# Performance work log

Measured on AMD Instinct MI355X. Metric: run time of the kernel, lower is better.

Reference implementation:

```python
import jax, jax.numpy as jnp
import numpy as np

B, T, D, H, L = 8, 64, 128, 4, 4
G = B * T            # 512 frame-graphs
NPG = 200            # nodes per graph
N = G * NPG          # 102400 nodes
E = 8 * N            # 819200 edges
FIN, HID = 2, 64
DH = D // H
NCLS = 2


def setup_inputs():
    key = jax.random.key(0)
    ks = jax.random.split(key, 16)
    w = lambda k, s: (jax.random.normal(k, s) * 0.05).astype(jnp.float32)
    x = jax.random.normal(ks[0], (N, FIN), dtype=jnp.float32)
    g = jax.random.randint(ks[1], (E,), 0, G)
    src = (g * NPG + jax.random.randint(ks[2], (E,), 0, NPG)).astype(jnp.int32)
    dst = (g * NPG + jax.random.randint(ks[3], (E,), 0, NPG)).astype(jnp.int32)
    node_graph = (jnp.arange(N) // NPG).astype(jnp.int32)
    return dict(
        x=x, edge_src=src, edge_dst=dst, node_graph=node_graph,
        gW1=w(ks[4], (FIN, HID)), gb1=jnp.zeros((HID,), jnp.float32),
        ln1g=jnp.ones((HID,), jnp.float32), ln1b=jnp.zeros((HID,), jnp.float32),
        gW2=w(ks[5], (HID, HID)), gb2=jnp.zeros((HID,), jnp.float32),
        ln2g=jnp.ones((HID,), jnp.float32), ln2b=jnp.zeros((HID,), jnp.float32),
        gW3=w(ks[6], (HID, D)), gb3=jnp.zeros((D,), jnp.float32),
        tWqkv=w(ks[7], (L, 3 * D, D)), tbqkv=jnp.zeros((L, 3 * D), jnp.float32),
        tWo=w(ks[8], (L, D, D)), tbo=jnp.zeros((L, D), jnp.float32),
        tg1=jnp.ones((L, D), jnp.float32), tb1=jnp.zeros((L, D), jnp.float32),
        tg2=jnp.ones((L, D), jnp.float32), tb2=jnp.zeros((L, D), jnp.float32),
        tWf1=w(ks[9], (L, 4 * D, D)), tbf1=jnp.zeros((L, 4 * D), jnp.float32),
        tWf2=w(ks[10], (L, D, 4 * D)), tbf2=jnp.zeros((L, D), jnp.float32),
        hW1=w(ks[11], (D // 2, D)), hb1=jnp.zeros((D // 2,), jnp.float32),
        hW2=w(ks[12], (NCLS, D // 2)), hb2=jnp.zeros((NCLS,), jnp.float32),
    )


def _ln(x, g, b, eps=1e-5):
    m = jnp.mean(x, -1, keepdims=True)
    v = jnp.var(x, -1, keepdims=True)
    return (x - m) * jax.lax.rsqrt(v + eps) * g + b


def _forward(x, edge_src, edge_dst, node_graph, gW1, gb1, ln1g, ln1b, gW2, gb2,
             ln2g, ln2b, gW3, gb3, tWqkv, tbqkv, tWo, tbo, tg1, tb1, tg2, tb2,
             tWf1, tbf1, tWf2, tbf2, hW1, hb1, hW2, hb2):
    # --- GCN encoder (PyG GCNConv: sym-normalized A with self loops) ---
    loops = jnp.arange(N, dtype=jnp.int32)
    src = jnp.concatenate([edge_src, loops])
    dst = jnp.concatenate([edge_dst, loops])
    deg = jnp.zeros((N,), x.dtype).at[dst].add(1.0)
    dinv = jax.lax.rsqrt(deg)
    norm = (dinv[src] * dinv[dst])[:, None]

    def gcn(h, W, b):
        h = h @ W  # transform first (smaller message dim when FIN < HID)
        return jax.ops.segment_sum(h[src] * norm, dst, num_segments=N) + b

    h = _ln(jax.nn.relu(gcn(x, gW1, gb1)), ln1g, ln1b)
    h = _ln(jax.nn.relu(gcn(h, gW2, gb2)), ln2g, ln2b)
    h = gcn(h, gW3, gb3)  # (N, D)

    # per-graph mean readout (replaces the python loop in the original)
    cnt = jax.ops.segment_sum(jnp.ones((N,), h.dtype), node_graph, num_segments=G)
    emb = jax.ops.segment_sum(h, node_graph, num_segments=G) / cnt[:, None]
    seq = emb.reshape(B, T, D)

    # --- sinusoidal positional encoding ---
    pos = jnp.arange(T, dtype=jnp.float32)[:, None]
    div = jnp.exp(jnp.arange(0, D, 2, dtype=jnp.float32) * (-np.log(10000.0) / D))
    pe = jnp.zeros((T, D), jnp.float32)
    pe = pe.at[:, 0::2].set(jnp.sin(pos * div)).at[:, 1::2].set(jnp.cos(pos * div))
    seq = seq + pe

    # --- TransformerEncoder (post-norm, relu FFN, batch_first) ---
    scale = 1.0 / np.sqrt(DH)
    for l in range(L):
        qkv = seq @ tWqkv[l].T + tbqkv[l]
        q, k, v = jnp.split(qkv, 3, axis=-1)
        q = q.reshape(B, T, H, DH).transpose(0, 2, 1, 3)
        k = k.reshape(B, T, H, DH).transpose(0, 2, 1, 3)
        v = v.reshape(B, T, H, DH).transpose(0, 2, 1, 3)
        att = jax.nn.softmax(jnp.einsum('bhqd,bhkd->bhqk', q, k) * scale, axis=-1)
        a = jnp.einsum('bhqk,bhkd->bhqd', att, v).transpose(0, 2, 1, 3).reshape(B, T, D)
        seq = _ln(seq + a @ tWo[l].T + tbo[l], tg1[l], tb1[l])
        f = jax.nn.relu(seq @ tWf1[l].T + tbf1[l]) @ tWf2[l].T + tbf2[l]
        seq = _ln(seq + f, tg2[l], tb2[l])

    pooled = jnp.mean(seq, axis=1)  # mask=None path -> plain temporal mean
    return jax.nn.relu(pooled @ hW1.T + hb1) @ hW2.T + hb2  # (B, NCLS)


def reference(x, edge_src, edge_dst, node_graph, gW1, gb1, ln1g, ln1b, gW2, gb2,
              ln2g, ln2b, gW3, gb3, tWqkv, tbqkv, tWo, tbo, tg1, tb1, tg2, tb2,
              tWf1, tbf1, tWf2, tbf2, hW1, hb1, hW2, hb2):
    return _forward(x, edge_src, edge_dst, node_graph, gW1, gb1, ln1g, ln1b,
                    gW2, gb2, ln2g, ln2b, gW3, gb3, tWqkv, tbqkv, tWo, tbo,
                    tg1, tb1, tg2, tb2, tWf1, tbf1, tWf2, tbf2, hW1, hb1, hW2, hb2)
```

## Files before the change

kernel.cpp:

```cpp
#include <hip/hip_runtime.h>

#define NN   102400
#define EE   819200
#define GG   512
#define NPG  200
#define DD   128
#define TT   64
#define BB   8
#define LL   4
#define ECHUNK 12800
#define SCAP 2560
#define NSLOT 16

typedef unsigned int uint;

static __device__ __forceinline__ void wave_sum64_2(float& a, float& b) {
#pragma unroll
    for (int off = 32; off > 0; off >>= 1) {
        a += __shfl_xor(a, off, 64);
        b += __shfl_xor(b, off, 64);
    }
}


__global__ __launch_bounds__(256) void k_a1(const int* __restrict__ src,
                                            int* __restrict__ hist) {
    __shared__ int h[GG];
    int tid = threadIdx.x;
    h[tid] = 0; h[tid + 256] = 0;
    __syncthreads();
    int base = blockIdx.x * ECHUNK;
#pragma unroll 2
    for (int it = 0; it < 50; ++it)
        atomicAdd(&h[src[base + it * 256 + tid] / NPG], 1);
    __syncthreads();
    hist[blockIdx.x * GG + tid] = h[tid];
    hist[blockIdx.x * GG + tid + 256] = h[tid + 256];
}

__global__ __launch_bounds__(512) void k_a2(const int* __restrict__ hist,
                                            int* __restrict__ off2,
                                            int* __restrict__ goff) {
    __shared__ int sm[GG];
    int g = threadIdx.x;
    int s = 0;
    for (int b = 0; b < 64; ++b) s += hist[b * GG + g];
    sm[g] = s;
    __syncthreads();
    for (int d = 1; d < GG; d <<= 1) {
        int v = (g >= d) ? sm[g - d] : 0;
        __syncthreads();
        sm[g] += v;
        __syncthreads();
    }
    int base = sm[g] - s;
    goff[g] = base;
    if (g == GG - 1) goff[GG] = sm[g];
    int run = base;
    for (int b = 0; b < 64; ++b) {
        off2[b * GG + g] = run;
        run += hist[b * GG + g];
    }
}

__global__ __launch_bounds__(256) void k_a3(const int* __restrict__ src,
                                            const int* __restrict__ dst,
                                            const int* __restrict__ off2,
                                            uint* __restrict__ gpack) {
    __shared__ int cur[GG];
    int tid = threadIdx.x;
    cur[tid] = off2[blockIdx.x * GG + tid];
    cur[tid + 256] = off2[blockIdx.x * GG + tid + 256];
    __syncthreads();
    int base = blockIdx.x * ECHUNK;
    for (int it = 0; it < 50; ++it) {
        int e = base + it * 256 + tid;
        int s = src[e], d = dst[e];
        int g = s / NPG;
        int pos = atomicAdd(&cur[g], 1);
        gpack[pos] = ((uint)(s - g * NPG) << 8) | (uint)(d - g * NPG);
    }
}

__global__ __launch_bounds__(256) void k_bsort(
    const float* __restrict__ x, const int* __restrict__ goff,
    const uint* __restrict__ gpack, const float* __restrict__ W1,
    const float* __restrict__ gb1, const float* __restrict__ lng,
    const float* __restrict__ lnb, uint2* __restrict__ slots,
    uint2* __restrict__ ovf, int* __restrict__ ovfcnt,
    float* __restrict__ wgtv, float* __restrict__ hout) {
    int g = ((blockIdx.x & 7) << 6) | (blockIdx.x >> 3);
    __shared__ float2 xs[NPG];
    __shared__ float2 aggl[NPG];
    __shared__ int cnt2[NPG];
    __shared__ int lnoff[NPG + 1];
    __shared__ int cur[NPG];
    __shared__ float rsq[NPG];
    __shared__ float cwl[NPG];
    __shared__ uint srec[SCAP];
    __shared__ int sm[256];
    __shared__ uint2 ovfl[128];
    __shared__ int ovfcur;
    int tid = threadIdx.x;
    int base = goff[g], E = goff[g + 1] - base;
    const float2* x2 = (const float2*)x;
    if (tid < NPG) { xs[tid] = x2[g * NPG + tid]; cnt2[tid] = 0; cwl[tid] = 0.f; }
    if (tid == 0) ovfcur = 0;
    __syncthreads();
    for (int i = tid; i < E; i += 256) atomicAdd(&cnt2[gpack[base + i] & 255u], 1);
    __syncthreads();
    int c = (tid < NPG) ? cnt2[tid] : 0;
    sm[tid] = c;
    __syncthreads();
    for (int d = 1; d < 256; d <<= 1) {
        int v = (tid >= d) ? sm[tid - d] : 0;
        __syncthreads();
        sm[tid] += v;
        __syncthreads();
    }
    if (tid < NPG) {
        lnoff[tid] = sm[tid] - c;
        cur[tid] = sm[tid] - c;
        rsq[tid] = rsqrtf((float)(c + 1));
    }
    if (tid == 0) lnoff[NPG] = E;
    __syncthreads();
    for (int i = tid; i < E; i += 256) {
        uint r = gpack[base + i];
        int pos = atomicAdd(&cur[r & 255u], 1);
        srec[pos] = r;
    }
    __syncthreads();
    for (int i = tid; i < E; i += 256) {
        uint r = srec[i];
        atomicAdd(&cwl[r >> 8], rsq[r >> 8] * rsq[r & 255u]);
    }
    __syncthreads();
    if (tid < NPG) {
        int e0 = lnoff[tid], En = lnoff[tid + 1] - e0;
        float rd = rsq[tid];
        float dv = rd * rd;
        uint2* op = &slots[(size_t)(g * NPG + tid) * NSLOT];
        op[0] = make_uint2((uint)(g * NPG + tid), __float_as_uint(dv));
        float ax = xs[tid].x * dv, ay = xs[tid].y * dv;
#pragma unroll
        for (int s = 1; s < NSLOT; ++s) {
            uint2 v;
            if (s - 1 < En) {
                uint r = srec[e0 + s - 1];
                int ls = r >> 8;
                float w = rsq[ls] * rd;
                v = make_uint2((uint)(g * NPG + ls), __float_as_uint(w));
                ax += xs[ls].x * w;
                ay += xs[ls].y * w;
            } else {
                v = make_uint2((uint)(g * NPG + tid), 0u);
            }
            op[s] = v;
        }
        for (int e = NSLOT - 1; e < En; ++e) {
            uint r = srec[e0 + e];
            int ls = r >> 8;
            float w = rsq[ls] * rd;
            ax += xs[ls].x * w;
            ay += xs[ls].y * w;
            int p = atomicAdd(&ovfcur, 1);
            if (p < 128)
                ovfl[p] = make_uint2(((uint)tid << 17) | (uint)(g * NPG + ls),
                                     __float_as_uint(w));
        }
        aggl[tid] = make_float2(ax, ay);
        wgtv[g * NPG + tid] = cwl[tid] + dv;
    }
    __syncthreads();
    int nov = ovfcur < 128 ? ovfcur : 128;
    if (tid == 0) ovfcnt[g] = nov;
    if (tid < nov) ovf[g * 128 + tid] = ovfl[tid];
    int lane = tid & 63, wid = tid >> 6;
    float w0 = W1[lane], w1 = W1[64 + lane];
    float gbj = gb1[lane], lgj = lng[lane], lbj = lnb[lane];
    for (int i = wid; i < NPG; i += 4) {
        float2 a = aggl[i];
        float u = fmaxf(a.x * w0 + a.y * w1 + gbj, 0.f);
        float s2 = u, q2 = u * u;
        wave_sum64_2(s2, q2);
        float mean = s2 * (1.f / 64.f);
        float var = q2 * (1.f / 64.f) - mean * mean;
        hout[(size_t)(g * NPG + i) * 64 + lane] = (u - mean) * rsqrtf(var + 1e-5f) * lgj + lbj;
    }
}


__global__ __launch_bounds__(256) void k_agg_lin_ln(
    const float* __restrict__ t, const float* __restrict__ W,
    const float* __restrict__ gb, const float* __restrict__ lng,
    const float* __restrict__ lnb, const uint2* __restrict__ slots,
    const uint2* __restrict__ ovf, const int* __restrict__ ovfcnt,
    float* __restrict__ hout) {
    int c = ((blockIdx.x & 7) << 8) | (blockIdx.x >> 3);
    int n0 = c * 50;
    int g = c >> 2, lbase = (c & 3) * 50;
    __shared__ float hs[50][64];
    __shared__ uint2 slt[50][NSLOT];
    int tid = threadIdx.x, lane = tid & 63, wid = tid >> 6;
    int grp = lane >> 4, fq = lane & 15;
    {
        const float4* s4 = (const float4*)&slots[(size_t)n0 * NSLOT];
        float4* d4 = (float4*)slt;
        for (int i = tid; i < 50 * NSLOT / 2; i += 256) d4[i] = s4[i];
    }
    __syncthreads();
    for (int i = wid; i < 50; i += 4) {
        float4 acc = make_float4(0.f, 0.f, 0.f, 0.f);
#pragma unroll
        for (int r = 0; r < 4; ++r) {
            uint2 s = slt[i][r * 4 + grp];
            float w = __uint_as_float(s.y);
            float4 tv = *(const float4*)&t[(size_t)s.x * 64 + fq * 4];
            acc.x += tv.x * w; acc.y += tv.y * w;
            acc.z += tv.z * w; acc.w += tv.w * w;
        }
        acc.x += __shfl_xor(acc.x, 16); acc.y += __shfl_xor(acc.y, 16);
        acc.z += __shfl_xor(acc.z, 16); acc.w += __shfl_xor(acc.w, 16);
        acc.x += __shfl_xor(acc.x, 32); acc.y += __shfl_xor(acc.y, 32);
        acc.z += __shfl_xor(acc.z, 32); acc.w += __shfl_xor(acc.w, 32);
        if (grp == 0) *(float4*)&hs[i][fq * 4] = acc;
    }
    __syncthreads();
    int nov = ovfcnt[g];
    if (nov && wid == 0) {
        for (int k = 0; k < nov; ++k) {
            uint2 r = ovf[g * 128 + k];
            int ld = r.x >> 17;
            if (ld >= lbase && ld < lbase + 50)
                hs[ld - lbase][lane] +=
                    t[(size_t)(r.x & 0x1FFFFu) * 64 + lane] * __uint_as_float(r.y);
        }
    }
    __syncthreads();
    float wreg[64];
#pragma unroll
    for (int k = 0; k < 64; ++k) wreg[k] = W[k * 64 + lane];
    float gbj = gb[lane], lgj = lng[lane], lbj = lnb[lane];
    for (int i = wid; i < 50; i += 4) {
        const float4* hrow = (const float4*)&hs[i][0];
        float a0 = 0.f, a1 = 0.f;
#pragma unroll
        for (int k4 = 0; k4 < 16; k4 += 2) {
            float4 h0 = hrow[k4], h1 = hrow[k4 + 1];
            a0 += h0.x * wreg[4 * k4] + h0.y * wreg[4 * k4 + 1] +
                  h0.z * wreg[4 * k4 + 2] + h0.w * wreg[4 * k4 + 3];
            a1 += h1.x * wreg[4 * k4 + 4] + h1.y * wreg[4 * k4 + 5] +
                  h1.z * wreg[4 * k4 + 6] + h1.w * wreg[4 * k4 + 7];
        }
        float u = fmaxf(a0 + a1 + gbj, 0.f);
        float s = u, q = u * u;
        wave_sum64_2(s, q);
        float mean = s * (1.f / 64.f);
        float var = q * (1.f / 64.f) - mean * mean;
        hout[(size_t)(n0 + i) * 64 + lane] = (u - mean) * rsqrtf(var + 1e-5f) * lgj + lbj;
    }
}

__global__ __launch_bounds__(256) void k_wpool_emb(
    const float* __restrict__ h2, const float* __restrict__ wgtv,
    const float* __restrict__ W3, const float* __restrict__ b3,
    float* __restrict__ seq) {
    int g = ((blockIdx.x & 7) << 6) | (blockIdx.x >> 3);
    int n0 = g * NPG;
    __shared__ float wgt[NPG];
    __shared__ float red[4][64];
    __shared__ float ps[64];
    int tid = threadIdx.x, lane = tid & 63, wid = tid >> 6;
    for (int i = tid; i < NPG; i += 256) wgt[i] = wgtv[n0 + i];
    __syncthreads();
    float acc = 0.f;
    for (int i = wid; i < NPG; i += 4)
        acc += h2[(size_t)(n0 + i) * 64 + lane] * wgt[i];
    red[wid][lane] = acc;
    __syncthreads();
    if (tid < 64)
        ps[tid] = (red[0][tid] + red[1][tid] + red[2][tid] + red[3][tid]) * (1.f / NPG);
    __syncthreads();
    if (tid < 128) {
        int d = tid;
        float a = b3[d];
#pragma unroll 8
        for (int k = 0; k < 64; ++k) a += ps[k] * W3[k * DD + d];
        float freq = expf((float)(d & ~1) * (-9.210340371976184f / 128.f));
        float ang = (float)(g & (TT - 1)) * freq;
        a += (d & 1) ? cosf(ang) : sinf(ang);
        seq[(size_t)g * DD + d] = a;
    }
}


__global__ __launch_bounds__(512) void k_qkv_attn(
    const float* __restrict__ seq, const float* __restrict__ Wqkv,
    const float* __restrict__ bqkv, float* __restrict__ abuf) {
    int b = blockIdx.x >> 2, h = blockIdx.x & 3;
    __shared__ float seqs[64][132];
    __shared__ float Qs[64][36], Ks[64][36], Vs[64][36];
    __shared__ float Ss[64][68];
    int tid = threadIdx.x;
    for (int i = tid; i < 64 * 32; i += 512) {
        int r = i >> 5, c = i & 31;
        float4 v = *(const float4*)&seq[(size_t)(b * 64 + r) * DD + c * 4];
        *(float4*)&seqs[r][c * 4] = v;
    }
    __syncthreads();
    {
        int r = tid & 63, jg = tid >> 6;
        float acc[12];
        int wrow[12];
#pragma unroll
        for (int i = 0; i < 12; ++i) {
            int jj = jg * 12 + i;
            int row = (jj < 32) ? (h * 32 + jj)
                    : (jj < 64) ? (128 + h * 32 + jj - 32)
                                : (256 + h * 32 + jj - 64);
            wrow[i] = row;
            acc[i] = bqkv[row];
        }
        for (int kc = 0; kc < 8; ++kc) {
            float4 s0 = *(const float4*)&seqs[r][kc * 16 + 0];
            float4 s1 = *(const float4*)&seqs[r][kc * 16 + 4];
            float4 s2 = *(const float4*)&seqs[r][kc * 16 + 8];
            float4 s3 = *(const float4*)&seqs[r][kc * 16 + 12];
#pragma unroll
            for (int i = 0; i < 12; ++i) {
                const float4* wp = (const float4*)&Wqkv[(size_t)wrow[i] * DD + kc * 16];
                float4 w0 = wp[0], w1 = wp[1], w2 = wp[2], w3 = wp[3];
                acc[i] += s0.x * w0.x + s0.y * w0.y + s0.z * w0.z + s0.w * w0.w +
                          s1.x * w1.x + s1.y * w1.y + s1.z * w1.z + s1.w * w1.w +
                          s2.x * w2.x + s2.y * w2.y + s2.z * w2.z + s2.w * w2.w +
                          s3.x * w3.x + s3.y * w3.y + s3.z * w3.z + s3.w * w3.w;
            }
        }
#pragma unroll
        for (int i = 0; i < 12; ++i) {
            int jj = jg * 12 + i;
            if (jj < 32) Qs[r][jj] = acc[i];
            else if (jj < 64) Ks[r][jj - 32] = acc[i];
            else Vs[r][jj - 64] = acc[i];
        }
    }
    __syncthreads();
    int q = tid >> 3, kg = tid & 7;
    const float scale = 0.17677669529663687f;
    float p[8];
    float mx = -1e30f;
#pragma unroll
    for (int kk = 0; kk < 8; ++kk) {
        int k = kg * 8 + kk;
        float a = 0.f;
#pragma unroll
        for (int dq = 0; dq < 8; ++dq) {
            float4 qv = *(const float4*)&Qs[q][dq * 4];
            float4 kv = *(const float4*)&Ks[k][dq * 4];
            a += qv.x * kv.x + qv.y * kv.y + qv.z * kv.z + qv.w * kv.w;
        }
        p[kk] = a * scale;
        mx = fmaxf(mx, p[kk]);
    }
    mx = fmaxf(mx, __shfl_xor(mx, 1));
    mx = fmaxf(mx, __shfl_xor(mx, 2));
    mx = fmaxf(mx, __shfl_xor(mx, 4));
    float ssum = 0.f;
#pragma unroll
    for (int kk = 0; kk < 8; ++kk) {
        p[kk] = expf(p[kk] - mx);
        ssum += p[kk];
    }
    ssum += __shfl_xor(ssum, 1);
    ssum += __shfl_xor(ssum, 2);
    ssum += __shfl_xor(ssum, 4);
    float inv = 1.f / ssum;
#pragma unroll
    for (int kk = 0; kk < 8; ++kk) Ss[q][kg * 8 + kk] = p[kk] * inv;
    __syncthreads();
    float4 o = make_float4(0.f, 0.f, 0.f, 0.f);
    for (int k = 0; k < 64; ++k) {
        float pw = Ss[q][k];
        float4 v = *(const float4*)&Vs[k][kg * 4];
        o.x += pw * v.x; o.y += pw * v.y; o.z += pw * v.z; o.w += pw * v.w;
    }
    *(float4*)&abuf[(size_t)(b * 64 + q) * DD + h * 32 + kg * 4] = o;
}

__global__ __launch_bounds__(128) void k_proj_ln(
    const float* __restrict__ abuf, const float* __restrict__ Wo,
    const float* __restrict__ bo, const float* __restrict__ g,
    const float* __restrict__ bl, float* __restrict__ seq) {
    int m = blockIdx.x, tid = threadIdx.x;
    __shared__ float arow[128];
    __shared__ float sred[2][2];
    arow[tid] = abuf[(size_t)m * DD + tid];
    __syncthreads();
    float acc = bo[tid];
    const float4* wr = (const float4*)&Wo[(size_t)tid * DD];
    const float4* ar = (const float4*)arow;
#pragma unroll
    for (int k = 0; k < 32; ++k) {
        float4 w = wr[k], a = ar[k];
        acc += a.x * w.x + a.y * w.y + a.z * w.z + a.w * w.w;
    }
    float u = seq[(size_t)m * DD + tid] + acc;
    float s = u, q2 = u * u;
    wave_sum64_2(s, q2);
    int wid = tid >> 6;
    if ((tid & 63) == 0) { sred[wid][0] = s; sred[wid][1] = q2; }
    __syncthreads();
    s = sred[0][0] + sred[1][0];
    q2 = sred[0][1] + sred[1][1];
    float mean = s * (1.f / 128.f);
    float var = q2 * (1.f / 128.f) - mean * mean;
    float rstd = rsqrtf(var + 1e-5f);
    seq[(size_t)m * DD + tid] = (u - mean) * rstd * g[tid] + bl[tid];
}

__global__ __launch_bounds__(256) void k_ffn_ln(
    const float* __restrict__ Wf1, const float* __restrict__ bf1,
    const float* __restrict__ Wf2, const float* __restrict__ bf2,
    const float* __restrict__ g, const float* __restrict__ bl,
    float* __restrict__ seq) {
    int m0 = blockIdx.x * 2, tid = threadIdx.x;
    __shared__ float srow[2][128];
    __shared__ float f1[2][512];
    __shared__ float pf[2][128];
    __shared__ float sred2[2][4];
    {
        int rr = tid >> 7, d = tid & 127;
        srow[rr][d] = seq[(size_t)(m0 + rr) * DD + d];
    }
    __syncthreads();
    const float4* s0 = (const float4*)srow[0];
    const float4* s1 = (const float4*)srow[1];
#pragma unroll
    for (int rep = 0; rep < 2; ++rep) {
        int o = tid + rep * 256;
        float bv = bf1[o];
        float a0 = bv, a1 = bv;
        const float4* wr = (const float4*)&Wf1[(size_t)o * DD];
#pragma unroll
        for (int k = 0; k < 32; ++k) {
            float4 w = wr[k];
            float4 x0 = s0[k], x1 = s1[k];
            a0 += x0.x * w.x + x0.y * w.y + x0.z * w.z + x0.w * w.w;
            a1 += x1.x * w.x + x1.y * w.y + x1.z * w.z + x1.w * w.w;
        }
        f1[0][o] = fmaxf(a0, 0.f);
        f1[1][o] = fmaxf(a1, 0.f);
    }
    __syncthreads();
    int d = tid & 127, half = tid >> 7;
    float b0 = half ? 0.f : bf2[d];
    float a0 = b0, a1 = b0;
    const float4* wr2 = (const float4*)&Wf2[(size_t)d * 512 + half * 256];
    const float4* f10 = (const float4*)&f1[0][half * 256];
    const float4* f11 = (const float4*)&f1[1][half * 256];
#pragma unroll
    for (int k = 0; k < 64; ++k) {
        float4 w = wr2[k];
        float4 x0 = f10[k], x1 = f11[k];
        a0 += x0.x * w.x + x0.y * w.y + x0.z * w.z + x0.w * w.w;
        a1 += x1.x * w.x + x1.y * w.y + x1.z * w.z + x1.w * w.w;
    }
    if (half) { pf[0][d] = a0; pf[1][d] = a1; }
    __syncthreads();
    float u0 = 0.f, u1 = 0.f;
    if (half == 0) {
        u0 = srow[0][d] + a0 + pf[0][d];
        u1 = srow[1][d] + a1 + pf[1][d];
        float s0_ = u0, q0_ = u0 * u0, s1_ = u1, q1_ = u1 * u1;
        wave_sum64_2(s0_, q0_);
        wave_sum64_2(s1_, q1_);
        int w_ = d >> 6;
        if ((d & 63) == 0) {
            sred2[w_][0] = s0_; sred2[w_][1] = q0_;
            sred2[w_][2] = s1_; sred2[w_][3] = q1_;
        }
    }
    __syncthreads();
    if (half == 0) {
        float S0 = sred2[0][0] + sred2[1][0], Q0 = sred2[0][1] + sred2[1][1];
        float S1 = sred2[0][2] + sred2[1][2], Q1 = sred2[0][3] + sred2[1][3];
        float mean0 = S0 * (1.f / 128.f);
        float var0 = Q0 * (1.f / 128.f) - mean0 * mean0;
        float rstd0 = rsqrtf(var0 + 1e-5f);
        float mean1 = S1 * (1.f / 128.f);
        float var1 = Q1 * (1.f / 128.f) - mean1 * mean1;
        float rstd1 = rsqrtf(var1 + 1e-5f);
        seq[(size_t)m0 * DD + d] = (u0 - mean0) * rstd0 * g[d] + bl[d];
        seq[(size_t)(m0 + 1) * DD + d] = (u1 - mean1) * rstd1 * g[d] + bl[d];
    }
}

__global__ __launch_bounds__(128) void k_head(
    const float* __restrict__ seq, const float* __restrict__ W1,
    const float* __restrict__ b1, const float* __restrict__ W2,
    const float* __restrict__ b2, float* __restrict__ out) {
    int b = blockIdx.x, t = threadIdx.x;
    __shared__ float pooled[DD];
    __shared__ float hid[64];
    float s = 0.f;
    for (int i = 0; i < TT; ++i) s += seq[(size_t)(b * TT + i) * DD + t];
    pooled[t] = s * (1.f / TT);
    __syncthreads();
    if (t < 64) {
        float a = b1[t];
        const float* wr = W1 + t * DD;
        for (int k = 0; k < DD; ++k) a += pooled[k] * wr[k];
        hid[t] = fmaxf(a, 0.f);
    }
    __syncthreads();
    if (t < 2) {
        float a = b2[t];
        const float* wr = W2 + t * 64;
        for (int k = 0; k < 64; ++k) a += hid[k] * wr[k];
        out[b * 2 + t] = a;
    }
}


extern "C" void kernel_launch(void* const* d_in, const int* in_sizes, int n_in,
                              void* d_out, int out_size, void* d_ws, size_t ws_size,
                              hipStream_t stream) {
    const float* x     = (const float*)d_in[0];
    const int*   esrc  = (const int*)d_in[1];
    const int*   edst  = (const int*)d_in[2];
    const float* gW1   = (const float*)d_in[4];
    const float* gb1   = (const float*)d_in[5];
    const float* ln1g  = (const float*)d_in[6];
    const float* ln1b  = (const float*)d_in[7];
    const float* gW2   = (const float*)d_in[8];
    const float* gb2   = (const float*)d_in[9];
    const float* ln2g  = (const float*)d_in[10];
    const float* ln2b  = (const float*)d_in[11];
    const float* gW3   = (const float*)d_in[12];
    const float* gb3   = (const float*)d_in[13];
    const float* tWqkv = (const float*)d_in[14];
    const float* tbqkv = (const float*)d_in[15];
    const float* tWo   = (const float*)d_in[16];
    const float* tbo   = (const float*)d_in[17];
    const float* tg1   = (const float*)d_in[18];
    const float* tb1   = (const float*)d_in[19];
    const float* tg2   = (const float*)d_in[20];
    const float* tb2   = (const float*)d_in[21];
    const float* tWf1  = (const float*)d_in[22];
    const float* tbf1  = (const float*)d_in[23];
    const float* tWf2  = (const float*)d_in[24];
    const float* tbf2  = (const float*)d_in[25];
    const float* hW1   = (const float*)d_in[26];
    const float* hb1   = (const float*)d_in[27];
    const float* hW2   = (const float*)d_in[28];
    const float* hb2   = (const float*)d_in[29];
    float* out = (float*)d_out;

    int*   hist   = (int*)d_ws;
    int*   off2   = hist + 64 * GG;
    int*   goff   = off2 + 64 * GG;
    uint*  gpack  = (uint*)(goff + 516);
    uint2* slots  = (uint2*)(gpack + EE);
    uint2* ovf    = slots + (size_t)NN * NSLOT;
    int*   ovfcnt = (int*)(ovf + GG * 128);
    float* wgtv   = (float*)(ovfcnt + GG);
    float* bufA = wgtv + NN;
    float* bufB = bufA + (size_t)NN * 64;
    float* seq  = bufB + (size_t)NN * 64;
    float* abuf = seq + GG * DD;

    k_a1<<<64, 256, 0, stream>>>(esrc, hist);
    k_a2<<<1, 512, 0, stream>>>(hist, off2, goff);
    k_a3<<<64, 256, 0, stream>>>(esrc, edst, off2, gpack);
    k_bsort<<<GG, 256, 0, stream>>>(x, goff, gpack, gW1, gb1, ln1g, ln1b,
                                    slots, ovf, ovfcnt, wgtv, bufA);

    k_agg_lin_ln<<<NN / 50, 256, 0, stream>>>(bufA, gW2, gb2, ln2g, ln2b,
                                              slots, ovf, ovfcnt, bufB);
    k_wpool_emb<<<GG, 256, 0, stream>>>(bufB, wgtv, gW3, gb3, seq);

    for (int l = 0; l < LL; l++) {
        k_qkv_attn<<<BB * 4, 512, 0, stream>>>(
            seq, tWqkv + (size_t)l * 384 * 128, tbqkv + l * 384, abuf);
        k_proj_ln<<<GG, 128, 0, stream>>>(
            abuf, tWo + (size_t)l * 128 * 128, tbo + l * 128,
            tg1 + l * 128, tb1 + l * 128, seq);
        k_ffn_ln<<<GG / 2, 256, 0, stream>>>(
            tWf1 + (size_t)l * 512 * 128, tbf1 + l * 512,
            tWf2 + (size_t)l * 128 * 512, tbf2 + l * 128,
            tg2 + l * 128, tb2 + l * 128, seq);
    }

    k_head<<<BB, DD, 0, stream>>>(seq, hW1, hb1, hW2, hb2, out);
}
```

Measured before the change: 392.8 us.

## Fuse attention output projection+LN into FFN+LN kernel per layer

Merges the per-row output-projection/residual/LayerNorm kernel into the FFN kernel, so each block of two rows computes Wo projection, LN1, FFN and LN2 without writing the intermediate seq to global memory. This removes one launch per transformer layer and a global round trip of the seq activations. It also adds a min-blocks occupancy hint to the GCN aggregation kernel. The second __syncthreads moves inside divergent if/else branches, which relies on AMD barrier semantics across branches.

```diff
diff --git a/kernel.cpp b/kernel.cpp
--- a/kernel.cpp
+++ b/kernel.cpp
@@ -191,7 +191,7 @@
 }
 
 
-__global__ __launch_bounds__(256) void k_agg_lin_ln(
+__global__ __launch_bounds__(256, 4) void k_agg_lin_ln(
     const float* __restrict__ t, const float* __restrict__ W,
     const float* __restrict__ gb, const float* __restrict__ lng,
     const float* __restrict__ lnb, const uint2* __restrict__ slots,
@@ -388,50 +388,45 @@
     *(float4*)&abuf[(size_t)(b * 64 + q) * DD + h * 32 + kg * 4] = o;
 }
 
-__global__ __launch_bounds__(128) void k_proj_ln(
+__global__ __launch_bounds__(256) void k_post(
     const float* __restrict__ abuf, const float* __restrict__ Wo,
-    const float* __restrict__ bo, const float* __restrict__ g,
-    const float* __restrict__ bl, float* __restrict__ seq) {
-    int m = blockIdx.x, tid = threadIdx.x;
-    __shared__ float arow[128];
-    __shared__ float sred[2][2];
-    arow[tid] = abuf[(size_t)m * DD + tid];
-    __syncthreads();
-    float acc = bo[tid];
-    const float4* wr = (const float4*)&Wo[(size_t)tid * DD];
-    const float4* ar = (const float4*)arow;
-#pragma unroll
-    for (int k = 0; k < 32; ++k) {
-        float4 w = wr[k], a = ar[k];
-        acc += a.x * w.x + a.y * w.y + a.z * w.z + a.w * w.w;
-    }
-    float u = seq[(size_t)m * DD + tid] + acc;
-    float s = u, q2 = u * u;
-    wave_sum64_2(s, q2);
-    int wid = tid >> 6;
-    if ((tid & 63) == 0) { sred[wid][0] = s; sred[wid][1] = q2; }
-    __syncthreads();
-    s = sred[0][0] + sred[1][0];
-    q2 = sred[0][1] + sred[1][1];
-    float mean = s * (1.f / 128.f);
-    float var = q2 * (1.f / 128.f) - mean * mean;
-    float rstd = rsqrtf(var + 1e-5f);
-    seq[(size_t)m * DD + tid] = (u - mean) * rstd * g[tid] + bl[tid];
-}
-
-__global__ __launch_bounds__(256) void k_ffn_ln(
-    const float* __restrict__ Wf1, const float* __restrict__ bf1,
-    const float* __restrict__ Wf2, const float* __restrict__ bf2,
-    const float* __restrict__ g, const float* __restrict__ bl,
-    float* __restrict__ seq) {
+    const float* __restrict__ bo, const float* __restrict__ g1,
+    const float* __restrict__ bl1, const float* __restrict__ Wf1,
+    const float* __restrict__ bf1, const float* __restrict__ Wf2,
+    const float* __restrict__ bf2, const float* __restrict__ g2,
+    const float* __restrict__ bl2, float* __restrict__ seq) {
     int m0 = blockIdx.x * 2, tid = threadIdx.x;
+    __shared__ float arow[2][128];
     __shared__ float srow[2][128];
     __shared__ float f1[2][512];
     __shared__ float pf[2][128];
+    __shared__ float sred[4][2];
     __shared__ float sred2[2][4];
+    int rr = tid >> 7, d0 = tid & 127;
+    arow[rr][d0] = abuf[(size_t)(m0 + rr) * DD + d0];
+    __syncthreads();
     {
-        int rr = tid >> 7, d = tid & 127;
-        srow[rr][d] = seq[(size_t)(m0 + rr) * DD + d];
+        float acc = bo[d0];
+        const float4* wr = (const float4*)&Wo[(size_t)d0 * DD];
+        const float4* ar = (const float4*)arow[rr];
+#pragma unroll
+        for (int k = 0; k < 32; ++k) {
+            float4 w = wr[k], a = ar[k];
+            acc += a.x * w.x + a.y * w.y + a.z * w.z + a.w * w.w;
+        }
+        float u = seq[(size_t)(m0 + rr) * DD + d0] + acc;
+        float s = u, q = u * u;
+        wave_sum64_2(s, q);
+        int wv = tid >> 6;
+        if ((tid & 63) == 0) { sred[wv][0] = s; sred[wv][1] = q; }
+        __syncthreads();
+        int wp = rr * 2;
+        s = sred[wp][0] + sred[wp + 1][0];
+        q = sred[wp][1] + sred[wp + 1][1];
+        float mean = s * (1.f / 128.f);
+        float var = q * (1.f / 128.f) - mean * mean;
+        float rstd = rsqrtf(var + 1e-5f);
+        srow[rr][d0] = (u - mean) * rstd * g1[d0] + bl1[d0];
     }
     __syncthreads();
     const float4* s0 = (const float4*)srow[0];
@@ -468,10 +463,9 @@
     }
     if (half) { pf[0][d] = a0; pf[1][d] = a1; }
     __syncthreads();
-    float u0 = 0.f, u1 = 0.f;
     if (half == 0) {
-        u0 = srow[0][d] + a0 + pf[0][d];
-        u1 = srow[1][d] + a1 + pf[1][d];
+        float u0 = srow[0][d] + a0 + pf[0][d];
+        float u1 = srow[1][d] + a1 + pf[1][d];
         float s0_ = u0, q0_ = u0 * u0, s1_ = u1, q1_ = u1 * u1;
         wave_sum64_2(s0_, q0_);
         wave_sum64_2(s1_, q1_);
@@ -480,9 +474,7 @@
             sred2[w_][0] = s0_; sred2[w_][1] = q0_;
             sred2[w_][2] = s1_; sred2[w_][3] = q1_;
         }
-    }
-    __syncthreads();
-    if (half == 0) {
+        __syncthreads();
         float S0 = sred2[0][0] + sred2[1][0], Q0 = sred2[0][1] + sred2[1][1];
         float S1 = sred2[0][2] + sred2[1][2], Q1 = sred2[0][3] + sred2[1][3];
         float mean0 = S0 * (1.f / 128.f);
@@ -491,8 +483,10 @@
         float mean1 = S1 * (1.f / 128.f);
         float var1 = Q1 * (1.f / 128.f) - mean1 * mean1;
         float rstd1 = rsqrtf(var1 + 1e-5f);
-        seq[(size_t)m0 * DD + d] = (u0 - mean0) * rstd0 * g[d] + bl[d];
-        seq[(size_t)(m0 + 1) * DD + d] = (u1 - mean1) * rstd1 * g[d] + bl[d];
+        seq[(size_t)m0 * DD + d] = (u0 - mean0) * rstd0 * g2[d] + bl2[d];
+        seq[(size_t)(m0 + 1) * DD + d] = (u1 - mean1) * rstd1 * g2[d] + bl2[d];
+    } else {
+        __syncthreads();
     }
 }
 
@@ -583,10 +577,9 @@
     for (int l = 0; l < LL; l++) {
         k_qkv_attn<<<BB * 4, 512, 0, stream>>>(
             seq, tWqkv + (size_t)l * 384 * 128, tbqkv + l * 384, abuf);
-        k_proj_ln<<<GG, 128, 0, stream>>>(
+        k_post<<<GG / 2, 256, 0, stream>>>(
             abuf, tWo + (size_t)l * 128 * 128, tbo + l * 128,
-            tg1 + l * 128, tb1 + l * 128, seq);
-        k_ffn_ln<<<GG / 2, 256, 0, stream>>>(
+            tg1 + l * 128, tb1 + l * 128,
             tWf1 + (size_t)l * 512 * 128, tbf1 + l * 512,
             tWf2 + (size_t)l * 128 * 512, tbf2 + l * 128,
             tg2 + l * 128, tb2 + l * 128, seq);
```

After: 393.0 us. No clear change (+0.1%).
